# Optimization experiments

Hardware: AMD Instinct MI355X
Metric: run time of the kernel (lower is better)

## Reference

```python
import jax, jax.numpy as jnp
import numpy as np

B, S, DIM = 2, 2048, 4096
NH, NKV, HD = 32, 8, 128  # q heads, kv heads, head dim
ROPE_THETA = 10000.0


def _rope_tables(seq_len, head_dim, dtype=jnp.float32):
    inv = 1.0 / (ROPE_THETA ** (jnp.arange(0, head_dim, 2, dtype=jnp.float32) / head_dim))
    t = jnp.arange(seq_len, dtype=jnp.float32)
    f = jnp.outer(t, inv)  # [S, HD/2]
    return jnp.cos(f).astype(dtype), jnp.sin(f).astype(dtype)


def setup_inputs() -> dict:
    key = jax.random.key(0)
    ks = jax.random.split(key, 5)
    cos, sin = _rope_tables(S, HD)
    scale = 0.02
    return {
        "x": jax.random.normal(ks[0], (B, S, DIM), jnp.float32),
        "start_pos": 0,
        "freqs_cos": cos,
        "freqs_sin": sin,
        "wq": jax.random.normal(ks[1], (DIM, NH * HD), jnp.float32) * scale,
        "wk": jax.random.normal(ks[2], (DIM, NKV * HD), jnp.float32) * scale,
        "wv": jax.random.normal(ks[3], (DIM, NKV * HD), jnp.float32) * scale,
        "wo": jax.random.normal(ks[4], (NH * HD, DIM), jnp.float32) * scale,
    }


def _apply_rope(x, cos, sin):
    # x: [B, S, H, D]; rotate interleaved (even, odd) pairs as complex numbers
    xr, xi = x[..., 0::2], x[..., 1::2]
    c = cos[None, :, None, :]
    s = sin[None, :, None, :]
    out_r = xr * c - xi * s
    out_i = xr * s + xi * c
    return jnp.stack([out_r, out_i], axis=-1).reshape(x.shape)


def reference(x, start_pos, freqs_cos, freqs_sin, wq, wk, wv, wo):
    b, s, _ = x.shape
    n_rep = NH // NKV
    xq = (x @ wq).reshape(b, s, NH, HD)
    xk = (x @ wk).reshape(b, s, NKV, HD)
    xv = (x @ wv).reshape(b, s, NKV, HD)
    xq = _apply_rope(xq, freqs_cos, freqs_sin)
    xk = _apply_rope(xk, freqs_cos, freqs_sin)
    # GQA: group q heads [B,S,NKV,n_rep,HD] against shared kv heads (no repeat_kv materialization)
    xqg = xq.reshape(b, s, NKV, n_rep, HD)
    scale = 1.0 / jnp.sqrt(jnp.asarray(HD, x.dtype))
    scores = jnp.einsum('bqhrd,bkhd->bhrqk', xqg, xk) * scale  # [B,NKV,n_rep,S,S]
    probs = jax.nn.softmax(scores, axis=-1)
    out = jnp.einsum('bhrqk,bkhd->bqhrd', probs, xv)  # [B,S,NKV,n_rep,HD]
    out = out.reshape(b, s, NH * HD)
    return out @ wo
```

## Files before the change

### kernel.cpp

```cpp
#include <hip/hip_runtime.h>

typedef unsigned short u16;
typedef unsigned int   u32;
typedef __attribute__((ext_vector_type(4))) float floatx4;
typedef __attribute__((ext_vector_type(8))) short shortx8;
typedef __attribute__((ext_vector_type(8))) u16   ushortx8;

#define B_   2
#define S_   2048
#define DIM_ 4096
#define NH_  32
#define NKV_ 8
#define HD_  128
#define MTOT (B_*S_)
#define NQKV (NH_*HD_ + 2*NKV_*HD_)
#define QSCALE 0.12753785735803168f
#define KSCALE 1.0f

typedef __attribute__((address_space(3))) u32 lds_u32;
typedef const __attribute__((address_space(1))) u32 gbl_u32;

__device__ inline u16 f2bf(float f) {
  __bf16 h = (__bf16)f;
  return __builtin_bit_cast(u16, h);
}
__device__ inline float bf2f(u16 u) {
  u32 x = ((u32)u) << 16;
  return __builtin_bit_cast(float, x);
}
__device__ inline shortx8 ldfrag(const u16* p) {
  return __builtin_bit_cast(shortx8, *(const uint4*)p);
}

__global__ __launch_bounds__(256) void cvt_f32_bf16(const float* __restrict__ src,
                                                    u16* __restrict__ dst) {
  int i = blockIdx.x * 256 + threadIdx.x;
  const float4* s4 = (const float4*)src;
  float4 a = s4[2*i], c = s4[2*i+1];
  ushortx8 o;
  o[0]=f2bf(a.x); o[1]=f2bf(a.y); o[2]=f2bf(a.z); o[3]=f2bf(a.w);
  o[4]=f2bf(c.x); o[5]=f2bf(c.y); o[6]=f2bf(c.z); o[7]=f2bf(c.w);
  *(ushortx8*)(dst + (size_t)i*8) = o;
}

__global__ __launch_bounds__(256) void transpose_cvt(const float* __restrict__ w,
                                                     u16* __restrict__ wt, int K, int N) {
  __shared__ float tile[32][33];
  int n0 = blockIdx.x * 32, k0 = blockIdx.y * 32;
  int tx = threadIdx.x & 31, ty = threadIdx.x >> 5;
#pragma unroll
  for (int i = 0; i < 4; i++) {
    int r = ty*4 + i;
    tile[r][tx] = w[(size_t)(k0 + r)*N + n0 + tx];
  }
  __syncthreads();
#pragma unroll
  for (int i = 0; i < 4; i++) {
    int n = ty*4 + i;
    wt[(size_t)(n0 + n)*K + k0 + tx] = f2bf(tile[tx][n]);
  }
}

template<int OUT_BF16>
__global__ __launch_bounds__(256) void gemm_bt(const u16* __restrict__ A,
                                               const u16* __restrict__ Bt,
                                               void* __restrict__ Cv,
                                               int M, int N, int K) {
  __shared__ u16 As[128*64];
  __shared__ u16 Bs[128*64];
  const int tid = threadIdx.x;
  const int w = tid >> 6, l = tid & 63, quad = l >> 4, c16 = l & 15;
  const int bm = blockIdx.y * 128, bn = blockIdx.x * 128;
  const int wm = (w & 1) * 64, wn = (w >> 1) * 64;
  const int drow = l >> 3;
  const int gchunk = (l & 7) ^ drow;
  const int dcol = gchunk * 8;
  floatx4 acc[4][4];
#pragma unroll
  for (int mi = 0; mi < 4; mi++)
#pragma unroll
    for (int ni = 0; ni < 4; ni++) acc[mi][ni] = floatx4{0.f,0.f,0.f,0.f};

  for (int k0 = 0; k0 < K; k0 += 64) {
    __syncthreads();
#pragma unroll
    for (int j = 0; j < 4; j++) {
      int row = w*32 + j*8 + drow;
      __builtin_amdgcn_global_load_lds(
          (gbl_u32*)(A + (size_t)(bm + row)*K + k0 + dcol),
          (lds_u32*)(As + (w*32 + j*8)*64), 16, 0, 0);
      __builtin_amdgcn_global_load_lds(
          (gbl_u32*)(Bt + (size_t)(bn + row)*K + k0 + dcol),
          (lds_u32*)(Bs + (w*32 + j*8)*64), 16, 0, 0);
    }
    __syncthreads();
#pragma unroll
    for (int ks = 0; ks < 2; ks++) {
      shortx8 af[4], bfr[4];
#pragma unroll
      for (int mi = 0; mi < 4; mi++) {
        int row = wm + mi*16 + c16;
        int ch  = (ks*4 + quad) ^ (row & 7);
        af[mi] = ldfrag(As + row*64 + ch*8);
      }
#pragma unroll
      for (int ni = 0; ni < 4; ni++) {
        int row = wn + ni*16 + c16;
        int ch  = (ks*4 + quad) ^ (row & 7);
        bfr[ni] = ldfrag(Bs + row*64 + ch*8);
      }
#pragma unroll
      for (int mi = 0; mi < 4; mi++)
#pragma unroll
        for (int ni = 0; ni < 4; ni++)
          acc[mi][ni] = __builtin_amdgcn_mfma_f32_16x16x32_bf16(af[mi], bfr[ni], acc[mi][ni], 0, 0, 0);
    }
  }
#pragma unroll
  for (int mi = 0; mi < 4; mi++)
#pragma unroll
    for (int i = 0; i < 4; i++) {
      int row = bm + wm + mi*16 + quad*4 + i;
#pragma unroll
      for (int ni = 0; ni < 4; ni++) {
        int col = bn + wn + ni*16 + c16;
        float v = acc[mi][ni][i];
        if (OUT_BF16) ((u16*)Cv)[(size_t)row*N + col] = f2bf(v);
        else          ((float*)Cv)[(size_t)row*N + col] = v;
      }
    }
}

__global__ __launch_bounds__(256) void rope_kernel(const u16* __restrict__ qkv,
                                                   const float* __restrict__ fc,
                                                   const float* __restrict__ fs,
                                                   u16* __restrict__ q_r,
                                                   u16* __restrict__ k_r) {
  u32 idx  = blockIdx.x * 256 + threadIdx.x;
  u32 t    = idx & 63;
  u32 rest = idx >> 6;
  u32 m    = rest / 40u;
  u32 hh   = rest - m*40u;
  u32 s    = m & (S_ - 1);
  float c  = fc[s*64 + t], sn = fs[s*64 + t];
  u32 src; u16* dst; u32 dstoff; float scale;
  if (hh < (u32)NH_) {
    src = m*NQKV + hh*HD_ + 2*t;  dst = q_r;  dstoff = m*(NH_*HD_) + hh*HD_ + 2*t;  scale = QSCALE;
  } else {
    u32 hk = hh - NH_;
    src = m*NQKV + NH_*HD_ + hk*HD_ + 2*t;  dst = k_r;  dstoff = m*(NKV_*HD_) + hk*HD_ + 2*t;  scale = KSCALE;
  }
  u32 pair = *(const u32*)(qkv + src);
  float xr = bf2f((u16)(pair & 0xffffu));
  float xi = bf2f((u16)(pair >> 16));
  float orr = (xr*c - xi*sn) * scale;
  float oii = (xr*sn + xi*c) * scale;
  u32 outp = (u32)f2bf(orr) | ((u32)f2bf(oii) << 16);
  *(u32*)(dst + dstoff) = outp;
}

__global__ __launch_bounds__(256) void v_transpose(const u16* __restrict__ qkv,
                                                   u16* __restrict__ vt) {
  __shared__ u16 tile[32][33];
  int bh = blockIdx.y; int b = bh >> 3, hk = bh & 7;
  int ts = (blockIdx.x & 63) * 32;
  int td = (blockIdx.x >> 6) * 32;
  int tx = threadIdx.x & 31, ty = threadIdx.x >> 5;
#pragma unroll
  for (int i = 0; i < 4; i++) {
    int r = ty*4 + i;
    tile[r][tx] = qkv[(size_t)(b*S_ + ts + r)*NQKV + (NH_*HD_ + NKV_*HD_) + hk*HD_ + td + tx];
  }
  __syncthreads();
#pragma unroll
  for (int i = 0; i < 4; i++) {
    int d = ty*4 + i;
    vt[((size_t)bh*HD_ + td + d)*S_ + ts + tx] = tile[tx][d];
  }
}

__global__ __launch_bounds__(256) void attn_kernel(const u16* __restrict__ Q,
                                                   const u16* __restrict__ Kr,
                                                   const u16* __restrict__ Vt,
                                                   u16* __restrict__ Out) {
  __shared__ u16 Qs[64*128];
  __shared__ u16 Ks[64*128];
  __shared__ u16 Vts[128*64];
  const int tid = threadIdx.x;
  const int w = tid >> 6, l = tid & 63, quad = l >> 4, c16 = l & 15;
  const int qt = blockIdx.x, h = blockIdx.y, b = blockIdx.z;
  const int hk = h >> 2;

  {
    const u16* qbase = Q + (size_t)(b*S_ + qt*64)*(NH_*HD_) + h*HD_;
#pragma unroll
    for (int j = 0; j < 4; j++) {
      int rowb = w*16 + j*4;
      int r = rowb + (l >> 4);
      int gch = (l & 15) ^ (r & 7);
      __builtin_amdgcn_global_load_lds(
          (gbl_u32*)(qbase + (size_t)r*(NH_*HD_) + gch*8),
          (lds_u32*)(Qs + rowb*128), 16, 0, 0);
    }
  }
  __syncthreads();
  shortx8 aq[4];
#pragma unroll
  for (int kk = 0; kk < 4; kk++)
    aq[kk] = ldfrag(Qs + (w*16 + c16)*128 + ((kk*4 + quad) ^ (c16 & 7))*8);

  floatx4 o[8];
#pragma unroll
  for (int f = 0; f < 8; f++) o[f] = floatx4{0.f,0.f,0.f,0.f};
  float mrow[4] = {-1e30f,-1e30f,-1e30f,-1e30f};
  float lrow[4] = {0.f,0.f,0.f,0.f};
  u16* pw = Qs + (w*16)*128;

  const u16* kbase = Kr + (size_t)(b*S_)*(NKV_*HD_) + hk*HD_;
  const u16* vbase = Vt + (size_t)(b*NKV_ + hk)*HD_*S_;

  for (int kt = 0; kt < S_/64; kt++) {
    __syncthreads();
#pragma unroll
    for (int j = 0; j < 4; j++) {
      int rowb = w*16 + j*4;
      int r = rowb + (l >> 4);
      int gch = (l & 15) ^ (r & 7);
      __builtin_amdgcn_global_load_lds(
          (gbl_u32*)(kbase + (size_t)(kt*64 + r)*(NKV_*HD_) + gch*8),
          (lds_u32*)(Ks + rowb*128), 16, 0, 0);
      int rowbv = w*32 + j*8;
      int rv = rowbv + (l >> 3);
      int gchv = (l & 7) ^ (rv & 7);
      __builtin_amdgcn_global_load_lds(
          (gbl_u32*)(vbase + (size_t)rv*S_ + kt*64 + gchv*8),
          (lds_u32*)(Vts + rowbv*64), 16, 0, 0);
    }
    __syncthreads();

    floatx4 sc[4];
#pragma unroll
    for (int nt = 0; nt < 4; nt++) sc[nt] = floatx4{0.f,0.f,0.f,0.f};
    __builtin_amdgcn_s_setprio(1);
#pragma unroll
    for (int kk = 0; kk < 4; kk++)
#pragma unroll
      for (int nt = 0; nt < 4; nt++) {
        int rowk = nt*16 + c16;
        shortx8 bk = ldfrag(Ks + rowk*128 + ((kk*4 + quad) ^ (c16 & 7))*8);
        sc[nt] = __builtin_amdgcn_mfma_f32_16x16x32_bf16(aq[kk], bk, sc[nt], 0, 0, 0);
      }
    __builtin_amdgcn_s_setprio(0);

    float mx4[4];
    float need = -1e30f;
#pragma unroll
    for (int i = 0; i < 4; i++) {
      float mx = fmaxf(fmaxf(sc[0][i], sc[1][i]), fmaxf(sc[2][i], sc[3][i]));
      mx = fmaxf(mx, __shfl_xor(mx, 1));
      mx = fmaxf(mx, __shfl_xor(mx, 2));
      mx = fmaxf(mx, __shfl_xor(mx, 4));
      mx = fmaxf(mx, __shfl_xor(mx, 8));
      mx4[i] = mx;
      need = fmaxf(need, mx - mrow[i]);
    }
    if (__all(need <= 8.0f)) {
#pragma unroll
      for (int i = 0; i < 4; i++) {
        float rs = 0.f;
#pragma unroll
        for (int nt = 0; nt < 4; nt++) {
          float p = __builtin_amdgcn_exp2f(sc[nt][i] - mrow[i]);
          sc[nt][i] = p; rs += p;
        }
        rs += __shfl_xor(rs, 1);
        rs += __shfl_xor(rs, 2);
        rs += __shfl_xor(rs, 4);
        rs += __shfl_xor(rs, 8);
        lrow[i] += rs;
      }
    } else {
      float alpha[4];
#pragma unroll
      for (int i = 0; i < 4; i++) {
        float mn = fmaxf(mrow[i], mx4[i]);
        float al = __builtin_amdgcn_exp2f(mrow[i] - mn);
        mrow[i] = mn;
        float rs = 0.f;
#pragma unroll
        for (int nt = 0; nt < 4; nt++) {
          float p = __builtin_amdgcn_exp2f(sc[nt][i] - mn);
          sc[nt][i] = p; rs += p;
        }
        rs += __shfl_xor(rs, 1);
        rs += __shfl_xor(rs, 2);
        rs += __shfl_xor(rs, 4);
        rs += __shfl_xor(rs, 8);
        lrow[i] = lrow[i]*al + rs;
        alpha[i] = al;
      }
#pragma unroll
      for (int f = 0; f < 8; f++)
#pragma unroll
        for (int i = 0; i < 4; i++) o[f][i] *= alpha[i];
    }

#pragma unroll
    for (int nt = 0; nt < 4; nt++)
#pragma unroll
      for (int i = 0; i < 4; i++) {
        int pr = quad*4 + i;
        int ch = (nt*2 + (c16 >> 3)) ^ (pr & 7);
        pw[pr*128 + ch*8 + (c16 & 7)] = f2bf(sc[nt][i]);
      }
    asm volatile("s_waitcnt lgkmcnt(0)" ::: "memory");

    __builtin_amdgcn_s_setprio(1);
#pragma unroll
    for (int kk2 = 0; kk2 < 2; kk2++) {
      shortx8 pf = ldfrag(pw + c16*128 + ((kk2*4 + quad) ^ (c16 & 7))*8);
#pragma unroll
      for (int f = 0; f < 8; f++) {
        int rv = f*16 + c16;
        shortx8 vf = ldfrag(Vts + rv*64 + ((kk2*4 + quad) ^ (rv & 7))*8);
        o[f] = __builtin_amdgcn_mfma_f32_16x16x32_bf16(pf, vf, o[f], 0, 0, 0);
      }
    }
    __builtin_amdgcn_s_setprio(0);
  }

#pragma unroll
  for (int i = 0; i < 4; i++) {
    int srow = qt*64 + w*16 + quad*4 + i;
    float inv = 1.f / lrow[i];
    size_t base = (size_t)(b*S_ + srow)*(NH_*HD_) + h*HD_;
#pragma unroll
    for (int f = 0; f < 8; f++)
      Out[base + f*16 + c16] = f2bf(o[f][i] * inv);
  }
}

extern "C" void kernel_launch(void* const* d_in, const int* in_sizes, int n_in,
                              void* d_out, int out_size, void* d_ws, size_t ws_size,
                              hipStream_t stream) {
  (void)in_sizes; (void)n_in; (void)out_size; (void)ws_size;
  const float* x  = (const float*)d_in[0];
  const float* fc = (const float*)d_in[2];
  const float* fs = (const float*)d_in[3];
  const float* wq = (const float*)d_in[4];
  const float* wk = (const float*)d_in[5];
  const float* wv = (const float*)d_in[6];
  const float* wo = (const float*)d_in[7];
  float* out = (float*)d_out;

  char* ws = (char*)d_ws;
  u16* xb    = (u16*)(ws);
  u16* wallt = (u16*)(ws + 33554432ull);
  u16* q_r   = (u16*)(ws + 33554432ull);
  u16* k_r   = (u16*)(ws + 67108864ull);
  u16* vt    = (u16*)(ws + 75497472ull);
  u16* wot   = (u16*)(ws + 83886080ull);
  u16* qkvp  = (u16*)(ws + 117440512ull);

  cvt_f32_bf16<<<8192, 256, 0, stream>>>(x, xb);
  transpose_cvt<<<dim3(128,128), 256, 0, stream>>>(wq, wallt, 4096, 4096);
  transpose_cvt<<<dim3(32,128),  256, 0, stream>>>(wk, wallt + (size_t)4096*4096, 4096, 1024);
  transpose_cvt<<<dim3(32,128),  256, 0, stream>>>(wv, wallt + (size_t)5120*4096, 4096, 1024);
  transpose_cvt<<<dim3(128,128), 256, 0, stream>>>(wo, wot, 4096, 4096);

  gemm_bt<1><<<dim3(48,32), 256, 0, stream>>>(xb, wallt, qkvp, MTOT, NQKV, DIM_);

  rope_kernel<<<40960, 256, 0, stream>>>(qkvp, fc, fs, q_r, k_r);
  v_transpose<<<dim3(256,16), 256, 0, stream>>>(qkvp, vt);

  attn_kernel<<<dim3(32,32,2), 256, 0, stream>>>(q_r, k_r, vt, xb);

  gemm_bt<0><<<dim3(32,32), 256, 0, stream>>>(xb, wot, out, MTOT, DIM_, 4096);
}
```

Before: 965.8 us.

## Double-buffer K/V tiles in attention and compute row sums via MFMA

The attention kernel now keeps two LDS buffers for K and V. It prefetches the next 64-key tile with global_load_lds while computing on the current one, which removes one barrier per iteration. The softmax row sum is no longer built from shuffle reductions; it is accumulated by an extra MFMA of the bf16 probabilities against a ones vector. The rescale check now uses one wave-wide max instead of per-row maxima. LDS use grows and the denominator now comes from bf16-rounded probabilities, which slightly changes the numerics.

```diff
diff --git a/kernel.cpp b/kernel.cpp
--- a/kernel.cpp
+++ b/kernel.cpp
@@ -184,12 +184,15 @@
                                                    const u16* __restrict__ Vt,
                                                    u16* __restrict__ Out) {
   __shared__ u16 Qs[64*128];
-  __shared__ u16 Ks[64*128];
-  __shared__ u16 Vts[128*64];
+  __shared__ u16 Ks[2][64*128];
+  __shared__ u16 Vts[2][128*64];
   const int tid = threadIdx.x;
   const int w = tid >> 6, l = tid & 63, quad = l >> 4, c16 = l & 15;
   const int qt = blockIdx.x, h = blockIdx.y, b = blockIdx.z;
   const int hk = h >> 2;
+
+  const u16* kbase = Kr + (size_t)(b*S_)*(NKV_*HD_) + hk*HD_;
+  const u16* vbase = Vt + (size_t)(b*NKV_ + hk)*HD_*S_;
 
   {
     const u16* qbase = Q + (size_t)(b*S_ + qt*64)*(NH_*HD_) + h*HD_;
@@ -203,40 +206,61 @@
           (lds_u32*)(Qs + rowb*128), 16, 0, 0);
     }
   }
+#pragma unroll
+  for (int j = 0; j < 4; j++) {
+    int rowb = w*16 + j*4;
+    int r = rowb + (l >> 4);
+    int gch = (l & 15) ^ (r & 7);
+    __builtin_amdgcn_global_load_lds(
+        (gbl_u32*)(kbase + (size_t)r*(NKV_*HD_) + gch*8),
+        (lds_u32*)(Ks[0] + rowb*128), 16, 0, 0);
+    int rowbv = w*32 + j*8;
+    int rv = rowbv + (l >> 3);
+    int gchv = (l & 7) ^ (rv & 7);
+    __builtin_amdgcn_global_load_lds(
+        (gbl_u32*)(vbase + (size_t)rv*S_ + gchv*8),
+        (lds_u32*)(Vts[0] + rowbv*64), 16, 0, 0);
+  }
   __syncthreads();
+
   shortx8 aq[4];
 #pragma unroll
   for (int kk = 0; kk < 4; kk++)
     aq[kk] = ldfrag(Qs + (w*16 + c16)*128 + ((kk*4 + quad) ^ (c16 & 7))*8);
 
+  shortx8 vones;
+#pragma unroll
+  for (int e = 0; e < 8; e++) vones[e] = (short)0x3F80;
+
   floatx4 o[8];
 #pragma unroll
   for (int f = 0; f < 8; f++) o[f] = floatx4{0.f,0.f,0.f,0.f};
+  floatx4 lacc = floatx4{0.f,0.f,0.f,0.f};
   float mrow[4] = {-1e30f,-1e30f,-1e30f,-1e30f};
-  float lrow[4] = {0.f,0.f,0.f,0.f};
   u16* pw = Qs + (w*16)*128;
 
-  const u16* kbase = Kr + (size_t)(b*S_)*(NKV_*HD_) + hk*HD_;
-  const u16* vbase = Vt + (size_t)(b*NKV_ + hk)*HD_*S_;
-
+  int cur = 0;
   for (int kt = 0; kt < S_/64; kt++) {
-    __syncthreads();
-#pragma unroll
-    for (int j = 0; j < 4; j++) {
-      int rowb = w*16 + j*4;
-      int r = rowb + (l >> 4);
-      int gch = (l & 15) ^ (r & 7);
-      __builtin_amdgcn_global_load_lds(
-          (gbl_u32*)(kbase + (size_t)(kt*64 + r)*(NKV_*HD_) + gch*8),
-          (lds_u32*)(Ks + rowb*128), 16, 0, 0);
-      int rowbv = w*32 + j*8;
-      int rv = rowbv + (l >> 3);
-      int gchv = (l & 7) ^ (rv & 7);
-      __builtin_amdgcn_global_load_lds(
-          (gbl_u32*)(vbase + (size_t)rv*S_ + kt*64 + gchv*8),
-          (lds_u32*)(Vts + rowbv*64), 16, 0, 0);
-    }
-    __syncthreads();
+    if (kt) __syncthreads();
+
+    if (kt + 1 < S_/64) {
+      int nb = cur ^ 1;
+#pragma unroll
+      for (int j = 0; j < 4; j++) {
+        int rowb = w*16 + j*4;
+        int r = rowb + (l >> 4);
+        int gch = (l & 15) ^ (r & 7);
+        __builtin_amdgcn_global_load_lds(
+            (gbl_u32*)(kbase + (size_t)((kt+1)*64 + r)*(NKV_*HD_) + gch*8),
+            (lds_u32*)(Ks[nb] + rowb*128), 16, 0, 0);
+        int rowbv = w*32 + j*8;
+        int rv = rowbv + (l >> 3);
+        int gchv = (l & 7) ^ (rv & 7);
+        __builtin_amdgcn_global_load_lds(
+            (gbl_u32*)(vbase + (size_t)rv*S_ + (kt+1)*64 + gchv*8),
+            (lds_u32*)(Vts[nb] + rowbv*64), 16, 0, 0);
+      }
+    }
 
     floatx4 sc[4];
 #pragma unroll
@@ -247,62 +271,50 @@
 #pragma unroll
       for (int nt = 0; nt < 4; nt++) {
         int rowk = nt*16 + c16;
-        shortx8 bk = ldfrag(Ks + rowk*128 + ((kk*4 + quad) ^ (c16 & 7))*8);
+        shortx8 bk = ldfrag(Ks[cur] + rowk*128 + ((kk*4 + quad) ^ (c16 & 7))*8);
         sc[nt] = __builtin_amdgcn_mfma_f32_16x16x32_bf16(aq[kk], bk, sc[nt], 0, 0, 0);
       }
     __builtin_amdgcn_s_setprio(0);
 
-    float mx4[4];
-    float need = -1e30f;
-#pragma unroll
-    for (int i = 0; i < 4; i++) {
-      float mx = fmaxf(fmaxf(sc[0][i], sc[1][i]), fmaxf(sc[2][i], sc[3][i]));
-      mx = fmaxf(mx, __shfl_xor(mx, 1));
-      mx = fmaxf(mx, __shfl_xor(mx, 2));
-      mx = fmaxf(mx, __shfl_xor(mx, 4));
-      mx = fmaxf(mx, __shfl_xor(mx, 8));
-      mx4[i] = mx;
-      need = fmaxf(need, mx - mrow[i]);
-    }
-    if (__all(need <= 8.0f)) {
-#pragma unroll
-      for (int i = 0; i < 4; i++) {
-        float rs = 0.f;
-#pragma unroll
-        for (int nt = 0; nt < 4; nt++) {
-          float p = __builtin_amdgcn_exp2f(sc[nt][i] - mrow[i]);
-          sc[nt][i] = p; rs += p;
-        }
-        rs += __shfl_xor(rs, 1);
-        rs += __shfl_xor(rs, 2);
-        rs += __shfl_xor(rs, 4);
-        rs += __shfl_xor(rs, 8);
-        lrow[i] += rs;
-      }
+    float mxall = fmaxf(fmaxf(fmaxf(sc[0][0], sc[0][1]), fmaxf(sc[0][2], sc[0][3])),
+                        fmaxf(fmaxf(sc[1][0], sc[1][1]), fmaxf(sc[1][2], sc[1][3])));
+    mxall = fmaxf(mxall,
+                  fmaxf(fmaxf(fmaxf(sc[2][0], sc[2][1]), fmaxf(sc[2][2], sc[2][3])),
+                        fmaxf(fmaxf(sc[3][0], sc[3][1]), fmaxf(sc[3][2], sc[3][3]))));
+    mxall = fmaxf(mxall, __shfl_xor(mxall, 1));
+    mxall = fmaxf(mxall, __shfl_xor(mxall, 2));
+    mxall = fmaxf(mxall, __shfl_xor(mxall, 4));
+    mxall = fmaxf(mxall, __shfl_xor(mxall, 8));
+    float mlow = fminf(fminf(mrow[0], mrow[1]), fminf(mrow[2], mrow[3]));
+
+    if (__all(mxall - mlow <= 8.0f)) {
+#pragma unroll
+      for (int i = 0; i < 4; i++)
+#pragma unroll
+        for (int nt = 0; nt < 4; nt++)
+          sc[nt][i] = __builtin_amdgcn_exp2f(sc[nt][i] - mrow[i]);
     } else {
       float alpha[4];
 #pragma unroll
       for (int i = 0; i < 4; i++) {
-        float mn = fmaxf(mrow[i], mx4[i]);
-        float al = __builtin_amdgcn_exp2f(mrow[i] - mn);
+        float mx = fmaxf(fmaxf(sc[0][i], sc[1][i]), fmaxf(sc[2][i], sc[3][i]));
+        mx = fmaxf(mx, __shfl_xor(mx, 1));
+        mx = fmaxf(mx, __shfl_xor(mx, 2));
+        mx = fmaxf(mx, __shfl_xor(mx, 4));
+        mx = fmaxf(mx, __shfl_xor(mx, 8));
+        float mn = fmaxf(mrow[i], mx);
+        alpha[i] = __builtin_amdgcn_exp2f(mrow[i] - mn);
         mrow[i] = mn;
-        float rs = 0.f;
-#pragma unroll
-        for (int nt = 0; nt < 4; nt++) {
-          float p = __builtin_amdgcn_exp2f(sc[nt][i] - mn);
-          sc[nt][i] = p; rs += p;
-        }
-        rs += __shfl_xor(rs, 1);
-        rs += __shfl_xor(rs, 2);
-        rs += __shfl_xor(rs, 4);
-        rs += __shfl_xor(rs, 8);
-        lrow[i] = lrow[i]*al + rs;
-        alpha[i] = al;
+#pragma unroll
+        for (int nt = 0; nt < 4; nt++)
+          sc[nt][i] = __builtin_amdgcn_exp2f(sc[nt][i] - mn);
       }
 #pragma unroll
       for (int f = 0; f < 8; f++)
 #pragma unroll
         for (int i = 0; i < 4; i++) o[f][i] *= alpha[i];
+#pragma unroll
+      for (int i = 0; i < 4; i++) lacc[i] *= alpha[i];
     }
 
 #pragma unroll
@@ -319,20 +331,22 @@
 #pragma unroll
     for (int kk2 = 0; kk2 < 2; kk2++) {
       shortx8 pf = ldfrag(pw + c16*128 + ((kk2*4 + quad) ^ (c16 & 7))*8);
+      lacc = __builtin_amdgcn_mfma_f32_16x16x32_bf16(pf, vones, lacc, 0, 0, 0);
 #pragma unroll
       for (int f = 0; f < 8; f++) {
         int rv = f*16 + c16;
-        shortx8 vf = ldfrag(Vts + rv*64 + ((kk2*4 + quad) ^ (rv & 7))*8);
+        shortx8 vf = ldfrag(Vts[cur] + rv*64 + ((kk2*4 + quad) ^ (rv & 7))*8);
         o[f] = __builtin_amdgcn_mfma_f32_16x16x32_bf16(pf, vf, o[f], 0, 0, 0);
       }
     }
     __builtin_amdgcn_s_setprio(0);
+    cur ^= 1;
   }
 
 #pragma unroll
   for (int i = 0; i < 4; i++) {
     int srow = qt*64 + w*16 + quad*4 + i;
-    float inv = 1.f / lrow[i];
+    float inv = 1.f / lacc[i];
     size_t base = (size_t)(b*S_ + srow)*(NH_*HD_) + h*HD_;
 #pragma unroll
     for (int f = 0; f < 8; f++)
```

After: 908.7 us. -5.9%, faster.
